# Optimization experiments

Measured on AMD Instinct MI355X. Metric: run time of the kernel, lower is better.

The kernel has to match this reference:

```python
import jax, jax.numpy as jnp
import numpy as np

N = 100000          # nodes
E = 1600000         # edges (before self-loops)
D_IN = 128          # graph.x feature dim
D_HID = 8           # hidden_dim = output_dim = 8 (hard-coded in __init__)
NUM_MASK = 10000    # int(0.1 * N), _mask_rate = 0.1
ATT_SLOPE = 0.2     # GATConv attention LeakyReLU slope
ACT_SLOPE = 0.01    # F.leaky_relu default slope


def setup_inputs() -> dict:
    key = jax.random.key(0)
    ks = jax.random.split(key, 16)
    x = jax.random.normal(ks[0], (N, D_IN), dtype=jnp.float32)
    edge_index = jax.random.randint(ks[1], (2, E), 0, N, dtype=jnp.int32)
    mask_nodes = jax.random.permutation(ks[2], N)[:NUM_MASK].astype(jnp.int32)
    s = lambda k, shape: jax.random.normal(k, shape, dtype=jnp.float32) * 0.1
    return {
        "x": x,
        "edge_index": edge_index,
        "mask_nodes": mask_nodes,
        "enc_mask_token": jnp.zeros((1, D_IN), dtype=jnp.float32),
        "enc_W": s(ks[3], (D_HID, D_IN)),
        "enc_a_src": s(ks[4], (D_HID,)),
        "enc_a_dst": s(ks[5], (D_HID,)),
        "enc_b": s(ks[6], (D_HID,)),
        "e2d_W": s(ks[7], (D_HID, D_HID)),
        "dec_W": s(ks[8], (D_IN, D_HID)),
        "dec_a_src": s(ks[9], (D_IN,)),
        "dec_a_dst": s(ks[10], (D_IN,)),
        "dec_b": s(ks[11], (D_IN,)),
    }


def gat_conv(x, W, a_src, a_dst, b, src, dst, n_nodes):
    """PyG GATConv, heads=1 (self-loops already appended to src/dst)."""
    h = x @ W.T                                  # [N, out]
    alpha_src = h @ a_src                        # [N]
    alpha_dst = h @ a_dst                        # [N]
    e = jax.nn.leaky_relu(alpha_src[src] + alpha_dst[dst], ATT_SLOPE)  # [E]
    # numerically-stable segment softmax over incoming edges per dst node
    m = jax.ops.segment_max(e, dst, num_segments=n_nodes)
    ex = jnp.exp(e - m[dst])
    denom = jax.ops.segment_sum(ex, dst, num_segments=n_nodes)
    alpha = ex / denom[dst]                      # [E]
    out = jax.ops.segment_sum(alpha[:, None] * h[src], dst, num_segments=n_nodes)
    return out + b


def reference(x, edge_index, mask_nodes, enc_mask_token,
              enc_W, enc_a_src, enc_a_dst, enc_b,
              e2d_W, dec_W, dec_a_src, dec_a_dst, dec_b):
    n = x.shape[0]
    # GATConv adds self-loops internally
    loops = jnp.arange(n, dtype=edge_index.dtype)
    src = jnp.concatenate([edge_index[0], loops])
    dst = jnp.concatenate([edge_index[1], loops])

    # encoding_mask_noise: out_x[mask]=0 then += enc_mask_token -> set to token
    use_x = x.at[mask_nodes].set(enc_mask_token[0])

    # encoder: GATConv(input_dim -> 8) + leaky_relu
    enc_rep = jax.nn.leaky_relu(
        gat_conv(use_x, enc_W, enc_a_src, enc_a_dst, enc_b, src, dst, n), ACT_SLOPE)

    rep = enc_rep @ e2d_W.T
    rep = rep.at[mask_nodes].set(0.0)            # re-mask before decoding

    # decoder: GATConv(8 -> input_dim) + leaky_relu
    recon = jax.nn.leaky_relu(
        gat_conv(rep, dec_W, dec_a_src, dec_a_dst, dec_b, src, dst, n), ACT_SLOPE)

    # cosine reconstruction loss on masked nodes (torch eps = 1e-8)
    x_init = x[mask_nodes]
    x_rec = recon[mask_nodes]
    eps = jnp.float32(1e-8)
    na = jnp.maximum(jnp.linalg.norm(x_rec, axis=-1), eps)
    nb = jnp.maximum(jnp.linalg.norm(x_init, axis=-1), eps)
    cos = jnp.sum(x_rec * x_init, axis=-1) / (na * nb)
    loss = 1.0 - jnp.mean(cos)
    return loss, enc_rep
```

## Files before the change

kernel.cpp:

```cpp
#include <hip/hip_runtime.h>

#define N_NODES 100000
#define N_EDGES 1600000
#define N_TOT   1700000
#define D_IN    128
#define D_H     8
#define N_MASK  10000

#define TS      256
#define NTE     391
#define CAPB    5760
#define TSD     64
#define NTD     157
#define CAPD    1536
#define NB_NODE 196
#define NB_BKT  831

__device__ __forceinline__ float lrelu(float v, float s){ return v > 0.f ? v : s*v; }

__device__ __forceinline__ float wave_sum(float v){
#pragma unroll
  for (int o = 32; o > 0; o >>= 1) v += __shfl_xor(v, o, 64);
  return v;
}

__global__ void k_ms(const int* __restrict__ mask_nodes, int* __restrict__ mask_slot,
                     const float* __restrict__ Wd, const float* __restrict__ a_src,
                     float* __restrict__ vvec){
  int i = blockIdx.x*blockDim.x + threadIdx.x;
  if (i < N_MASK) mask_slot[mask_nodes[i]] = i;
  if (blockIdx.x == 0 && threadIdx.x < D_H){
    float s = 0.f;
    for (int j = 0; j < D_IN; ++j) s += a_src[j] * Wd[j*D_H + threadIdx.x];
    vvec[threadIdx.x] = s;
  }
}

__global__ void __launch_bounds__(512) k_pre(
    const float* __restrict__ x, const float* __restrict__ token,
    const float* __restrict__ W, const float* __restrict__ a_src,
    const float* __restrict__ a_dst, const int* __restrict__ mask_slot,
    const int* __restrict__ ei,
    float* __restrict__ h1, float* __restrict__ as1, float* __restrict__ ad1,
    int* __restrict__ gcur_enc, int* __restrict__ gcur_dec,
    unsigned* __restrict__ be, unsigned* __restrict__ bd){
  __shared__ float smem[1104];
  if (blockIdx.x < NB_NODE){
    float* Ws = smem;
    float* sa = smem + D_H*D_IN;
    float* sd = sa + D_H;
    for (int t = threadIdx.x; t < D_H*D_IN; t += 512) Ws[t] = W[t];
    if (threadIdx.x < D_H)            sa[threadIdx.x] = a_src[threadIdx.x];
    else if (threadIdx.x < 2*D_H)     sd[threadIdx.x - D_H] = a_dst[threadIdx.x - D_H];
    __syncthreads();
    int wid = blockIdx.x*512 + threadIdx.x;
    if (wid >= N_NODES) return;
    const float* row = (mask_slot[wid] >= 0) ? token : (x + (size_t)wid*D_IN);
    float acc[D_H];
#pragma unroll
    for (int j = 0; j < D_H; ++j) acc[j] = 0.f;
#pragma unroll 8
    for (int i = 0; i < D_IN/4; ++i){
      float4 xc = *(const float4*)(row + 4*i);
#pragma unroll
      for (int j = 0; j < D_H; ++j){
        float4 wv = *(const float4*)(Ws + j*D_IN + 4*i);
        acc[j] += xc.x*wv.x + xc.y*wv.y + xc.z*wv.z + xc.w*wv.w;
      }
    }
    float as = 0.f, ad = 0.f;
#pragma unroll
    for (int j = 0; j < D_H; ++j){ as += acc[j]*sa[j]; ad += acc[j]*sd[j]; }
    float4* hp = (float4*)(h1 + (size_t)wid*D_H);
    hp[0] = make_float4(acc[0], acc[1], acc[2], acc[3]);
    hp[1] = make_float4(acc[4], acc[5], acc[6], acc[7]);
    as1[wid] = as; ad1[wid] = ad;
  } else {
    int* h_enc    = (int*)smem;
    int* base_enc = h_enc + NTE;
    int* h_dec    = base_enc + NTE;
    int* base_dec = h_dec + NTD;
    int tid = threadIdx.x;
    if (tid < NTE){ h_enc[tid] = 0; }
    if (tid < NTD){ h_dec[tid] = 0; }
    __syncthreads();
    int t0 = (blockIdx.x - NB_NODE)*2048;
    int s[4], d[4], sl[4];
#pragma unroll
    for (int k = 0; k < 4; ++k){
      int t = t0 + tid + k*512;
      s[k] = -1;
      if (t < N_TOT){
        if (t < N_EDGES){ s[k] = ei[t]; d[k] = ei[N_EDGES + t]; }
        else            { s[k] = t - N_EDGES; d[k] = s[k]; }
        sl[k] = mask_slot[d[k]];
        atomicAdd(&h_enc[d[k] >> 8], 1);
        if (sl[k] >= 0) atomicAdd(&h_dec[sl[k] >> 6], 1);
      }
    }
    __syncthreads();
    if (tid < NTE){ base_enc[tid] = atomicAdd(&gcur_enc[tid], h_enc[tid]); h_enc[tid] = 0; }
    if (tid < NTD){ base_dec[tid] = atomicAdd(&gcur_dec[tid], h_dec[tid]); h_dec[tid] = 0; }
    __syncthreads();
#pragma unroll
    for (int k = 0; k < 4; ++k){
      if (s[k] >= 0){
        int b = d[k] >> 8, loc = d[k] & 255;
        int idx = base_enc[b] + atomicAdd(&h_enc[b], 1);
        if (idx < CAPB) be[(size_t)b*CAPB + idx] = ((unsigned)s[k] << 8) | (unsigned)loc;
        if (sl[k] >= 0){
          int bs = sl[k] >> 6, locs = sl[k] & 63;
          int i2 = base_dec[bs] + atomicAdd(&h_dec[bs], 1);
          if (i2 < CAPD) bd[(size_t)bs*CAPD + i2] = ((unsigned)s[k] << 6) | (unsigned)locs;
        }
      }
    }
  }
}

__global__ void __launch_bounds__(512) k_agg_enc(const unsigned* __restrict__ be,
                          const int* __restrict__ gcur_enc,
                          const float* __restrict__ as1, const float* __restrict__ ad1,
                          const float* __restrict__ h1,
                          const float* __restrict__ enc_b, const float* __restrict__ e2dW,
                          const int* __restrict__ mask_slot, const float* __restrict__ v,
                          float* __restrict__ out_rep, float* __restrict__ rep,
                          float* __restrict__ ex2){
  __shared__ unsigned sorted[CAPB];
  __shared__ int hist[TS], off[TS], cur[TS];
  __shared__ float lad[TS];
  __shared__ float comb[TS*9];
  int tau = blockIdx.x, tid = threadIdx.x;
  int gb = tau*TS;
  if (tid < TS){
    hist[tid] = 0;
    int g = gb + tid; lad[tid] = (g < N_NODES) ? ad1[g] : 0.f;
  }
  __syncthreads();
  int n = min(gcur_enc[tau], CAPB);
  const unsigned* bb = be + (size_t)tau*CAPB;
  for (int i = tid; i < n; i += 512) atomicAdd(&hist[bb[i] & 255], 1);
  __syncthreads();
  if (tid < TS) off[tid] = hist[tid];
  __syncthreads();
#pragma unroll
  for (int s2 = 1; s2 < TS; s2 <<= 1){
    int vv = 0;
    if (tid < TS && tid >= s2) vv = off[tid - s2];
    __syncthreads();
    if (tid < TS) off[tid] += vv;
    __syncthreads();
  }
  if (tid < TS) cur[tid] = off[tid] - hist[tid];
  __syncthreads();
  for (int i = tid; i < n; i += 512){
    unsigned w = bb[i];
    int pos = atomicAdd(&cur[w & 255], 1);
    sorted[pos] = w;
  }
  __syncthreads();
  int c = tid & 255, half = tid >> 8;
  int start = off[c] - hist[c], deg = hist[c];
  int mid = start + ((deg + 1) >> 1), end = start + deg;
  int k0 = half ? mid : start, k1 = half ? end : mid;
  float adv = lad[c];
  float acc[9];
#pragma unroll
  for (int j = 0; j < 9; ++j) acc[j] = 0.f;
  int k = k0;
  for (; k + 2 <= k1; k += 2){
    unsigned w0 = sorted[k], w1 = sorted[k+1];
    int sA = w0 >> 8, sB = w1 >> 8;
    float asA = as1[sA], asB = as1[sB];
    float4 haA = *(const float4*)(h1 + (size_t)sA*D_H);
    float4 hbA = *(const float4*)(h1 + (size_t)sA*D_H + 4);
    float4 haB = *(const float4*)(h1 + (size_t)sB*D_H);
    float4 hbB = *(const float4*)(h1 + (size_t)sB*D_H + 4);
    float exA = __expf(lrelu(asA + adv, 0.2f));
    float exB = __expf(lrelu(asB + adv, 0.2f));
    acc[0] += exA*haA.x; acc[1] += exA*haA.y; acc[2] += exA*haA.z; acc[3] += exA*haA.w;
    acc[4] += exA*hbA.x; acc[5] += exA*hbA.y; acc[6] += exA*hbA.z; acc[7] += exA*hbA.w;
    acc[8] += exA;
    acc[0] += exB*haB.x; acc[1] += exB*haB.y; acc[2] += exB*haB.z; acc[3] += exB*haB.w;
    acc[4] += exB*hbB.x; acc[5] += exB*hbB.y; acc[6] += exB*hbB.z; acc[7] += exB*hbB.w;
    acc[8] += exB;
  }
  if (k < k1){
    unsigned w = sorted[k];
    int s = w >> 8;
    float as = as1[s];
    float4 ha = *(const float4*)(h1 + (size_t)s*D_H);
    float4 hb = *(const float4*)(h1 + (size_t)s*D_H + 4);
    float ex = __expf(lrelu(as + adv, 0.2f));
    acc[0] += ex*ha.x; acc[1] += ex*ha.y; acc[2] += ex*ha.z; acc[3] += ex*ha.w;
    acc[4] += ex*hb.x; acc[5] += ex*hb.y; acc[6] += ex*hb.z; acc[7] += ex*hb.w;
    acc[8] += ex;
  }
  if (half){
#pragma unroll
    for (int j = 0; j < 9; ++j) comb[c*9 + j] = acc[j];
  }
  __syncthreads();
  if (!half){
    int i = gb + c;
    if (i < N_NODES){
#pragma unroll
      for (int j = 0; j < 9; ++j) acc[j] += comb[c*9 + j];
      float inv = 1.0f / acc[8];
      float er[D_H];
#pragma unroll
      for (int j = 0; j < D_H; ++j){
        er[j] = lrelu(acc[j]*inv + enc_b[j], 0.01f);
        out_rep[(size_t)i*D_H + j] = er[j];
      }
      bool masked = mask_slot[i] >= 0;
      float as = 0.f;
      float rv[D_H];
#pragma unroll
      for (int kk = 0; kk < D_H; ++kk){
        float t = 0.f;
#pragma unroll
        for (int j = 0; j < D_H; ++j) t += er[j]*e2dW[kk*D_H + j];
        t = masked ? 0.f : t;
        rv[kk] = t;
        as += t * v[kk];
      }
      float4* rp = (float4*)(rep + (size_t)i*D_H);
      rp[0] = make_float4(rv[0], rv[1], rv[2], rv[3]);
      rp[1] = make_float4(rv[4], rv[5], rv[6], rv[7]);
      ex2[i] = __expf(lrelu(as, 0.2f));
    }
  }
}

__global__ void __launch_bounds__(512) k_agg_dec(const unsigned* __restrict__ bd,
                          const int* __restrict__ gcur_dec,
                          const float* __restrict__ ex2, const float* __restrict__ rep,
                          const float* __restrict__ Wd, const float* __restrict__ dec_b,
                          const int* __restrict__ mask_nodes, const float* __restrict__ x,
                          float* __restrict__ cos_sum, int* __restrict__ ticket,
                          float* __restrict__ out){
  __shared__ unsigned sorted[CAPD];
  __shared__ int hist[TSD], off[TSD], cur[TSD];
  __shared__ float comb[TSD*9];
  __shared__ float Wt[D_H*D_IN];
  __shared__ float wsum[8];
  int sg = blockIdx.x, tid = threadIdx.x;
  if (tid < TSD) hist[tid] = 0;
  for (int t = tid; t < D_H*D_IN; t += 512) Wt[(t & 7)*D_IN + (t >> 3)] = Wd[t];
  __syncthreads();
  int n = min(gcur_dec[sg], CAPD);
  const unsigned* bb = bd + (size_t)sg*CAPD;
  for (int i = tid; i < n; i += 512) atomicAdd(&hist[bb[i] & 63], 1);
  __syncthreads();
  if (tid < TSD) off[tid] = hist[tid];
  __syncthreads();
#pragma unroll
  for (int s2 = 1; s2 < TSD; s2 <<= 1){
    int vv = 0;
    if (tid < TSD && tid >= s2) vv = off[tid - s2];
    __syncthreads();
    if (tid < TSD) off[tid] += vv;
    __syncthreads();
  }
  if (tid < TSD) cur[tid] = off[tid] - hist[tid];
  __syncthreads();
  for (int i = tid; i < n; i += 512){
    unsigned w = bb[i];
    int pos = atomicAdd(&cur[w & 63], 1);
    sorted[pos] = w;
  }
  __syncthreads();
  int c = tid >> 3, part = tid & 7;
  int start = off[c] - hist[c], deg = hist[c], end = start + deg;
  float acc[9];
#pragma unroll
  for (int j = 0; j < 9; ++j) acc[j] = 0.f;
  int k = start + part;
  for (; k + 8 < end; k += 16){
    unsigned w0 = sorted[k], w1 = sorted[k+8];
    int sA = w0 >> 6, sB = w1 >> 6;
    float eA = ex2[sA], eB = ex2[sB];
    float4 raA = *(const float4*)(rep + (size_t)sA*D_H);
    float4 rbA = *(const float4*)(rep + (size_t)sA*D_H + 4);
    float4 raB = *(const float4*)(rep + (size_t)sB*D_H);
    float4 rbB = *(const float4*)(rep + (size_t)sB*D_H + 4);
    acc[0] += eA*raA.x; acc[1] += eA*raA.y; acc[2] += eA*raA.z; acc[3] += eA*raA.w;
    acc[4] += eA*rbA.x; acc[5] += eA*rbA.y; acc[6] += eA*rbA.z; acc[7] += eA*rbA.w;
    acc[8] += eA;
    acc[0] += eB*raB.x; acc[1] += eB*raB.y; acc[2] += eB*raB.z; acc[3] += eB*raB.w;
    acc[4] += eB*rbB.x; acc[5] += eB*rbB.y; acc[6] += eB*rbB.z; acc[7] += eB*rbB.w;
    acc[8] += eB;
  }
  if (k < end){
    unsigned w = sorted[k];
    int s = w >> 6;
    float E = ex2[s];
    float4 ra = *(const float4*)(rep + (size_t)s*D_H);
    float4 rb = *(const float4*)(rep + (size_t)s*D_H + 4);
    acc[0] += E*ra.x; acc[1] += E*ra.y; acc[2] += E*ra.z; acc[3] += E*ra.w;
    acc[4] += E*rb.x; acc[5] += E*rb.y; acc[6] += E*rb.z; acc[7] += E*rb.w;
    acc[8] += E;
  }
#pragma unroll
  for (int j = 0; j < 9; ++j){
    acc[j] += __shfl_xor(acc[j], 1, 64);
    acc[j] += __shfl_xor(acc[j], 2, 64);
    acc[j] += __shfl_xor(acc[j], 4, 64);
  }
  if (part == 0){
#pragma unroll
    for (int j = 0; j < 9; ++j) comb[c*9 + j] = acc[j];
  }
  __syncthreads();
  int wv = tid >> 6, lane = tid & 63;
  float accv = 0.f;
  for (int sl = wv; sl < TSD; sl += 8){
    int slot = sg*TSD + sl;
    if (slot >= N_MASK) break;
    const float* a = comb + sl*9;
    float inv = 1.0f / a[8];
    int node = mask_nodes[slot];
    float dot = 0.f, na = 0.f, nb = 0.f;
#pragma unroll
    for (int hh = 0; hh < 2; ++hh){
      int f = lane + 64*hh;
      float r = dec_b[f];
#pragma unroll
      for (int kk = 0; kk < D_H; ++kk) r += a[kk]*inv*Wt[kk*D_IN + f];
      r = lrelu(r, 0.01f);
      float xi = x[(size_t)node*D_IN + f];
      dot += r*xi; na += r*r; nb += xi*xi;
    }
    dot = wave_sum(dot); na = wave_sum(na); nb = wave_sum(nb);
    if (lane == 0) accv += dot / (fmaxf(sqrtf(na), 1e-8f)*fmaxf(sqrtf(nb), 1e-8f));
  }
  if (lane == 0) wsum[wv] = accv;
  __syncthreads();
  if (tid == 0){
    float b = 0.f;
#pragma unroll
    for (int q = 0; q < 8; ++q) b += wsum[q];
    atomicAdd(cos_sum, b);
    __threadfence();
    int t = atomicAdd(ticket, 1);
    if (t == gridDim.x - 1){
      float cc = atomicAdd(cos_sum, 0.0f);
      out[0] = 1.0f - cc / (float)N_MASK;
    }
  }
}

extern "C" void kernel_launch(void* const* d_in, const int* in_sizes, int n_in,
                              void* d_out, int out_size, void* d_ws, size_t ws_size,
                              hipStream_t stream){
  const float* x          = (const float*)d_in[0];
  const int*   ei         = (const int*)  d_in[1];
  const int*   mask_nodes = (const int*)  d_in[2];
  const float* token      = (const float*)d_in[3];
  const float* enc_W      = (const float*)d_in[4];
  const float* enc_as     = (const float*)d_in[5];
  const float* enc_ad     = (const float*)d_in[6];
  const float* enc_b      = (const float*)d_in[7];
  const float* e2d_W      = (const float*)d_in[8];
  const float* dec_W      = (const float*)d_in[9];
  const float* dec_as     = (const float*)d_in[10];
  const float* dec_b      = (const float*)d_in[12];
  float* out = (float*)d_out;

  char* w = (char*)d_ws;
  size_t off = 0;
  auto alloc = [&](size_t bytes)->char*{ char* p = w + off; off += (bytes + 255)/256*256; return p; };
  int*   gcur_enc = (int*)  alloc(NTE*4);
  int*   gcur_dec = (int*)  alloc(NTD*4);
  float* cos_sum  = (float*)alloc(4);
  int*   ticket   = (int*)  alloc(4);
  size_t zero_bytes = off;
  int*      mask_slot = (int*)     alloc((size_t)N_NODES*4);
  unsigned* be        = (unsigned*)alloc((size_t)NTE*CAPB*4);
  unsigned* bd        = (unsigned*)alloc((size_t)NTD*CAPD*4);
  float*    h1        = (float*)   alloc((size_t)N_NODES*D_H*4);
  float*    as1       = (float*)   alloc((size_t)N_NODES*4);
  float*    ad1       = (float*)   alloc((size_t)N_NODES*4);
  float*    rep       = (float*)   alloc((size_t)N_NODES*D_H*4);
  float*    ex2       = (float*)   alloc((size_t)N_NODES*4);
  float*    vvec      = (float*)   alloc(64);

  hipMemsetAsync(d_ws, 0, zero_bytes, stream);
  hipMemsetAsync(mask_slot, 0xFF, (size_t)N_NODES*4, stream);

  k_ms      <<<(N_MASK + 255)/256, 256, 0, stream>>>(mask_nodes, mask_slot, dec_W, dec_as, vvec);
  k_pre     <<<NB_NODE + NB_BKT, 512, 0, stream>>>(x, token, enc_W, enc_as, enc_ad, mask_slot,
                                                   ei, h1, as1, ad1, gcur_enc, gcur_dec, be, bd);
  k_agg_enc <<<NTE, 512, 0, stream>>>(be, gcur_enc, as1, ad1, h1, enc_b, e2d_W, mask_slot,
                                      vvec, out + 1, rep, ex2);
  k_agg_dec <<<NTD, 512, 0, stream>>>(bd, gcur_dec, ex2, rep, dec_W, dec_b, mask_nodes, x,
                                      cos_sum, ticket, out);
}
```

Measured before the change: 94.53 us.

## Split encoder projection across 8 lanes per node and replace memsets with init kernel

The encoder linear projection now assigns eight threads per node, each loading a 16-float slice of the row with coalesced float4 reads, then reduces the partial dot products with cross-lane shuffles. The block count for node work grows accordingly. Separately, the two hipMemsetAsync calls are replaced by a single small init kernel that sets mask_slot and the counters. This targets uncoalesced per-thread row reads and launch overhead, at the cost of more blocks and extra shuffles.

```diff
diff --git a/kernel.cpp b/kernel.cpp
--- a/kernel.cpp
+++ b/kernel.cpp
@@ -13,7 +13,7 @@
 #define TSD     64
 #define NTD     157
 #define CAPD    1536
-#define NB_NODE 196
+#define NB_NODE 1563
 #define NB_BKT  831
 
 __device__ __forceinline__ float lrelu(float v, float s){ return v > 0.f ? v : s*v; }
@@ -22,6 +22,18 @@
 #pragma unroll
   for (int o = 32; o > 0; o >>= 1) v += __shfl_xor(v, o, 64);
   return v;
+}
+
+__global__ void k_init(int* __restrict__ mask_slot, int* __restrict__ gcur_enc,
+                       int* __restrict__ gcur_dec, float* __restrict__ cos_sum,
+                       int* __restrict__ ticket){
+  int i = blockIdx.x*blockDim.x + threadIdx.x;
+  if (i < N_NODES) mask_slot[i] = -1;
+  if (blockIdx.x == 0){
+    if (threadIdx.x < NTE) gcur_enc[threadIdx.x] = 0;
+    if (threadIdx.x < NTD) gcur_dec[threadIdx.x] = 0;
+    if (threadIdx.x == 0){ cos_sum[0] = 0.f; ticket[0] = 0; }
+  }
 }
 
 __global__ void k_ms(const int* __restrict__ mask_nodes, int* __restrict__ mask_slot,
@@ -53,28 +65,46 @@
     if (threadIdx.x < D_H)            sa[threadIdx.x] = a_src[threadIdx.x];
     else if (threadIdx.x < 2*D_H)     sd[threadIdx.x - D_H] = a_dst[threadIdx.x - D_H];
     __syncthreads();
-    int wid = blockIdx.x*512 + threadIdx.x;
-    if (wid >= N_NODES) return;
-    const float* row = (mask_slot[wid] >= 0) ? token : (x + (size_t)wid*D_IN);
+    int p = threadIdx.x & 7;
+    int node = blockIdx.x*64 + (threadIdx.x >> 3);
+    if (node >= N_NODES) return;
+    const float* row = (mask_slot[node] >= 0) ? token : (x + (size_t)node*D_IN);
+    const float* rp = row + p*16;
+    float4 xa = *(const float4*)(rp);
+    float4 xb = *(const float4*)(rp + 4);
+    float4 xc = *(const float4*)(rp + 8);
+    float4 xd = *(const float4*)(rp + 12);
     float acc[D_H];
 #pragma unroll
-    for (int j = 0; j < D_H; ++j) acc[j] = 0.f;
-#pragma unroll 8
-    for (int i = 0; i < D_IN/4; ++i){
-      float4 xc = *(const float4*)(row + 4*i);
-#pragma unroll
-      for (int j = 0; j < D_H; ++j){
-        float4 wv = *(const float4*)(Ws + j*D_IN + 4*i);
-        acc[j] += xc.x*wv.x + xc.y*wv.y + xc.z*wv.z + xc.w*wv.w;
-      }
-    }
-    float as = 0.f, ad = 0.f;
-#pragma unroll
-    for (int j = 0; j < D_H; ++j){ as += acc[j]*sa[j]; ad += acc[j]*sd[j]; }
-    float4* hp = (float4*)(h1 + (size_t)wid*D_H);
-    hp[0] = make_float4(acc[0], acc[1], acc[2], acc[3]);
-    hp[1] = make_float4(acc[4], acc[5], acc[6], acc[7]);
-    as1[wid] = as; ad1[wid] = ad;
+    for (int j = 0; j < D_H; ++j){
+      const float* wj = Ws + j*D_IN + p*16;
+      float4 wa = *(const float4*)(wj);
+      float4 wb = *(const float4*)(wj + 4);
+      float4 wc = *(const float4*)(wj + 8);
+      float4 wd = *(const float4*)(wj + 12);
+      acc[j] = xa.x*wa.x + xa.y*wa.y + xa.z*wa.z + xa.w*wa.w
+             + xb.x*wb.x + xb.y*wb.y + xb.z*wb.z + xb.w*wb.w
+             + xc.x*wc.x + xc.y*wc.y + xc.z*wc.z + xc.w*wc.w
+             + xd.x*wd.x + xd.y*wd.y + xd.z*wd.z + xd.w*wd.w;
+    }
+#pragma unroll
+    for (int j = 0; j < D_H; ++j){
+      acc[j] += __shfl_xor(acc[j], 1, 64);
+      acc[j] += __shfl_xor(acc[j], 2, 64);
+      acc[j] += __shfl_xor(acc[j], 4, 64);
+    }
+    h1[(size_t)node*D_H + p] = acc[p];
+    if (p == 0){
+      float as = 0.f;
+#pragma unroll
+      for (int j = 0; j < D_H; ++j) as += acc[j]*sa[j];
+      as1[node] = as;
+    } else if (p == 1){
+      float ad = 0.f;
+#pragma unroll
+      for (int j = 0; j < D_H; ++j) ad += acc[j]*sd[j];
+      ad1[node] = ad;
+    }
   } else {
     int* h_enc    = (int*)smem;
     int* base_enc = h_enc + NTE;
@@ -375,7 +405,6 @@
   int*   gcur_dec = (int*)  alloc(NTD*4);
   float* cos_sum  = (float*)alloc(4);
   int*   ticket   = (int*)  alloc(4);
-  size_t zero_bytes = off;
   int*      mask_slot = (int*)     alloc((size_t)N_NODES*4);
   unsigned* be        = (unsigned*)alloc((size_t)NTE*CAPB*4);
   unsigned* bd        = (unsigned*)alloc((size_t)NTD*CAPD*4);
@@ -386,9 +415,7 @@
   float*    ex2       = (float*)   alloc((size_t)N_NODES*4);
   float*    vvec      = (float*)   alloc(64);
 
-  hipMemsetAsync(d_ws, 0, zero_bytes, stream);
-  hipMemsetAsync(mask_slot, 0xFF, (size_t)N_NODES*4, stream);
-
+  k_init    <<<(N_NODES + 511)/512, 512, 0, stream>>>(mask_slot, gcur_enc, gcur_dec, cos_sum, ticket);
   k_ms      <<<(N_MASK + 255)/256, 256, 0, stream>>>(mask_nodes, mask_slot, dec_W, dec_as, vvec);
   k_pre     <<<NB_NODE + NB_BKT, 512, 0, stream>>>(x, token, enc_W, enc_as, enc_ad, mask_slot,
                                                    ei, h1, as1, ad1, gcur_enc, gcur_dec, be, bd);
```

Result: slower. 98.29 us (+4.0%).

## Replace block-local histogram bucketing with direct padded global atomics

Applied to the files above, without the earlier changes.

The edge-bucketing blocks no longer build a per-block shared-memory histogram and reserve ranges with one global atomic per bucket. Instead each edge does its own global atomicAdd on a bucket counter, and the counters are padded to 16 ints apart to avoid false sharing. The two memsets are replaced by a single init kernel. This removes two block barriers and the two-pass structure, but raises global atomic traffic to about 1.7M contended atomics on 391 counters.

```diff
diff --git a/kernel.cpp b/kernel.cpp
--- a/kernel.cpp
+++ b/kernel.cpp
@@ -15,6 +15,7 @@
 #define CAPD    1536
 #define NB_NODE 196
 #define NB_BKT  831
+#define CPAD    16
 
 __device__ __forceinline__ float lrelu(float v, float s){ return v > 0.f ? v : s*v; }
 
@@ -22,6 +23,16 @@
 #pragma unroll
   for (int o = 32; o > 0; o >>= 1) v += __shfl_xor(v, o, 64);
   return v;
+}
+
+__global__ void k_init(int* __restrict__ mask_slot, int* __restrict__ gcur_enc,
+                       int* __restrict__ gcur_dec, float* __restrict__ cos_sum,
+                       int* __restrict__ ticket){
+  int i = blockIdx.x*blockDim.x + threadIdx.x;
+  if (i < N_NODES) mask_slot[i] = -1;
+  if (i < NTE*CPAD) gcur_enc[i] = 0;
+  if (i < NTD*CPAD) gcur_dec[i] = 0;
+  if (i == 0){ cos_sum[0] = 0.f; ticket[0] = 0; }
 }
 
 __global__ void k_ms(const int* __restrict__ mask_nodes, int* __restrict__ mask_slot,
@@ -44,7 +55,7 @@
     float* __restrict__ h1, float* __restrict__ as1, float* __restrict__ ad1,
     int* __restrict__ gcur_enc, int* __restrict__ gcur_dec,
     unsigned* __restrict__ be, unsigned* __restrict__ bd){
-  __shared__ float smem[1104];
+  __shared__ float smem[D_H*D_IN + 2*D_H];
   if (blockIdx.x < NB_NODE){
     float* Ws = smem;
     float* sa = smem + D_H*D_IN;
@@ -76,42 +87,22 @@
     hp[1] = make_float4(acc[4], acc[5], acc[6], acc[7]);
     as1[wid] = as; ad1[wid] = ad;
   } else {
-    int* h_enc    = (int*)smem;
-    int* base_enc = h_enc + NTE;
-    int* h_dec    = base_enc + NTE;
-    int* base_dec = h_dec + NTD;
-    int tid = threadIdx.x;
-    if (tid < NTE){ h_enc[tid] = 0; }
-    if (tid < NTD){ h_dec[tid] = 0; }
-    __syncthreads();
     int t0 = (blockIdx.x - NB_NODE)*2048;
-    int s[4], d[4], sl[4];
 #pragma unroll
     for (int k = 0; k < 4; ++k){
-      int t = t0 + tid + k*512;
-      s[k] = -1;
+      int t = t0 + threadIdx.x + k*512;
       if (t < N_TOT){
-        if (t < N_EDGES){ s[k] = ei[t]; d[k] = ei[N_EDGES + t]; }
-        else            { s[k] = t - N_EDGES; d[k] = s[k]; }
-        sl[k] = mask_slot[d[k]];
-        atomicAdd(&h_enc[d[k] >> 8], 1);
-        if (sl[k] >= 0) atomicAdd(&h_dec[sl[k] >> 6], 1);
-      }
-    }
-    __syncthreads();
-    if (tid < NTE){ base_enc[tid] = atomicAdd(&gcur_enc[tid], h_enc[tid]); h_enc[tid] = 0; }
-    if (tid < NTD){ base_dec[tid] = atomicAdd(&gcur_dec[tid], h_dec[tid]); h_dec[tid] = 0; }
-    __syncthreads();
-#pragma unroll
-    for (int k = 0; k < 4; ++k){
-      if (s[k] >= 0){
-        int b = d[k] >> 8, loc = d[k] & 255;
-        int idx = base_enc[b] + atomicAdd(&h_enc[b], 1);
-        if (idx < CAPB) be[(size_t)b*CAPB + idx] = ((unsigned)s[k] << 8) | (unsigned)loc;
-        if (sl[k] >= 0){
-          int bs = sl[k] >> 6, locs = sl[k] & 63;
-          int i2 = base_dec[bs] + atomicAdd(&h_dec[bs], 1);
-          if (i2 < CAPD) bd[(size_t)bs*CAPD + i2] = ((unsigned)s[k] << 6) | (unsigned)locs;
+        int s, d;
+        if (t < N_EDGES){ s = ei[t]; d = ei[N_EDGES + t]; }
+        else            { s = t - N_EDGES; d = s; }
+        int sl = mask_slot[d];
+        int b = d >> 8, loc = d & 255;
+        int idx = atomicAdd(&gcur_enc[b*CPAD], 1);
+        if (idx < CAPB) be[(size_t)b*CAPB + idx] = ((unsigned)s << 8) | (unsigned)loc;
+        if (sl >= 0){
+          int bs = sl >> 6, locs = sl & 63;
+          int i2 = atomicAdd(&gcur_dec[bs*CPAD], 1);
+          if (i2 < CAPD) bd[(size_t)bs*CAPD + i2] = ((unsigned)s << 6) | (unsigned)locs;
         }
       }
     }
@@ -137,7 +128,7 @@
     int g = gb + tid; lad[tid] = (g < N_NODES) ? ad1[g] : 0.f;
   }
   __syncthreads();
-  int n = min(gcur_enc[tau], CAPB);
+  int n = min(gcur_enc[tau*CPAD], CAPB);
   const unsigned* bb = be + (size_t)tau*CAPB;
   for (int i = tid; i < n; i += 512) atomicAdd(&hist[bb[i] & 255], 1);
   __syncthreads();
@@ -249,7 +240,7 @@
   if (tid < TSD) hist[tid] = 0;
   for (int t = tid; t < D_H*D_IN; t += 512) Wt[(t & 7)*D_IN + (t >> 3)] = Wd[t];
   __syncthreads();
-  int n = min(gcur_dec[sg], CAPD);
+  int n = min(gcur_dec[sg*CPAD], CAPD);
   const unsigned* bb = bd + (size_t)sg*CAPD;
   for (int i = tid; i < n; i += 512) atomicAdd(&hist[bb[i] & 63], 1);
   __syncthreads();
@@ -371,11 +362,10 @@
   char* w = (char*)d_ws;
   size_t off = 0;
   auto alloc = [&](size_t bytes)->char*{ char* p = w + off; off += (bytes + 255)/256*256; return p; };
-  int*   gcur_enc = (int*)  alloc(NTE*4);
-  int*   gcur_dec = (int*)  alloc(NTD*4);
+  int*   gcur_enc = (int*)  alloc((size_t)NTE*CPAD*4);
+  int*   gcur_dec = (int*)  alloc((size_t)NTD*CPAD*4);
   float* cos_sum  = (float*)alloc(4);
   int*   ticket   = (int*)  alloc(4);
-  size_t zero_bytes = off;
   int*      mask_slot = (int*)     alloc((size_t)N_NODES*4);
   unsigned* be        = (unsigned*)alloc((size_t)NTE*CAPB*4);
   unsigned* bd        = (unsigned*)alloc((size_t)NTD*CAPD*4);
@@ -386,9 +376,7 @@
   float*    ex2       = (float*)   alloc((size_t)N_NODES*4);
   float*    vvec      = (float*)   alloc(64);
 
-  hipMemsetAsync(d_ws, 0, zero_bytes, stream);
-  hipMemsetAsync(mask_slot, 0xFF, (size_t)N_NODES*4, stream);
-
+  k_init    <<<(N_NODES + 511)/512, 512, 0, stream>>>(mask_slot, gcur_enc, gcur_dec, cos_sum, ticket);
   k_ms      <<<(N_MASK + 255)/256, 256, 0, stream>>>(mask_nodes, mask_slot, dec_W, dec_as, vvec);
   k_pre     <<<NB_NODE + NB_BKT, 512, 0, stream>>>(x, token, enc_W, enc_as, enc_ad, mask_slot,
                                                    ei, h1, as1, ad1, gcur_enc, gcur_dec, be, bd);
```

Result: slower. 205.2 us (+117.1%).

## Handle self-loops analytically, replace memsets with init kernel, unroll gather by four

Applied to the files above, without the earlier changes.

Self-loop edges are no longer written into the bucket arrays. The encoder adds each node's self-loop term directly after its edge reduction, and the decoder adds 1 to the softmax denominator, since the masked rep is zero. Two hipMemsetAsync calls become one small init kernel, and the encoder gather loop is unrolled from two edges per step to four to expose more memory-level parallelism. This cuts the bucketing and sorting work and one launch of overhead. The decoder shortcut depends on the self-loop contribution for a masked node being exactly an exp of 1 with a zero rep value.

```diff
diff --git a/kernel.cpp b/kernel.cpp
--- a/kernel.cpp
+++ b/kernel.cpp
@@ -2,7 +2,6 @@
 
 #define N_NODES 100000
 #define N_EDGES 1600000
-#define N_TOT   1700000
 #define D_IN    128
 #define D_H     8
 #define N_MASK  10000
@@ -14,7 +13,8 @@
 #define NTD     157
 #define CAPD    1536
 #define NB_NODE 196
-#define NB_BKT  831
+#define EPB     2048
+#define NB_BKT  782
 
 __device__ __forceinline__ float lrelu(float v, float s){ return v > 0.f ? v : s*v; }
 
@@ -22,6 +22,16 @@
 #pragma unroll
   for (int o = 32; o > 0; o >>= 1) v += __shfl_xor(v, o, 64);
   return v;
+}
+
+__global__ void k_init(int* __restrict__ mask_slot, int* __restrict__ gcur_enc,
+                       int* __restrict__ gcur_dec, float* __restrict__ cos_sum,
+                       int* __restrict__ ticket){
+  int i = blockIdx.x*blockDim.x + threadIdx.x;
+  if (i < N_NODES) mask_slot[i] = -1;
+  if (i < NTE) gcur_enc[i] = 0;
+  if (i < NTD) gcur_dec[i] = 0;
+  if (i == 0){ cos_sum[0] = 0.f; ticket[0] = 0; }
 }
 
 __global__ void k_ms(const int* __restrict__ mask_nodes, int* __restrict__ mask_slot,
@@ -44,10 +54,10 @@
     float* __restrict__ h1, float* __restrict__ as1, float* __restrict__ ad1,
     int* __restrict__ gcur_enc, int* __restrict__ gcur_dec,
     unsigned* __restrict__ be, unsigned* __restrict__ bd){
-  __shared__ float smem[1104];
+  __shared__ int smem[1104];
   if (blockIdx.x < NB_NODE){
-    float* Ws = smem;
-    float* sa = smem + D_H*D_IN;
+    float* Ws = (float*)smem;
+    float* sa = Ws + D_H*D_IN;
     float* sd = sa + D_H;
     for (int t = threadIdx.x; t < D_H*D_IN; t += 512) Ws[t] = W[t];
     if (threadIdx.x < D_H)            sa[threadIdx.x] = a_src[threadIdx.x];
@@ -76,23 +86,22 @@
     hp[1] = make_float4(acc[4], acc[5], acc[6], acc[7]);
     as1[wid] = as; ad1[wid] = ad;
   } else {
-    int* h_enc    = (int*)smem;
+    int* h_enc    = smem;
     int* base_enc = h_enc + NTE;
     int* h_dec    = base_enc + NTE;
     int* base_dec = h_dec + NTD;
     int tid = threadIdx.x;
-    if (tid < NTE){ h_enc[tid] = 0; }
-    if (tid < NTD){ h_dec[tid] = 0; }
-    __syncthreads();
-    int t0 = (blockIdx.x - NB_NODE)*2048;
+    if (tid < NTE) h_enc[tid] = 0;
+    if (tid < NTD) h_dec[tid] = 0;
+    __syncthreads();
+    int t0 = (blockIdx.x - NB_NODE)*EPB;
     int s[4], d[4], sl[4];
 #pragma unroll
     for (int k = 0; k < 4; ++k){
       int t = t0 + tid + k*512;
       s[k] = -1;
-      if (t < N_TOT){
-        if (t < N_EDGES){ s[k] = ei[t]; d[k] = ei[N_EDGES + t]; }
-        else            { s[k] = t - N_EDGES; d[k] = s[k]; }
+      if (t < N_EDGES){
+        s[k] = ei[t]; d[k] = ei[N_EDGES + t];
         sl[k] = mask_slot[d[k]];
         atomicAdd(&h_enc[d[k] >> 8], 1);
         if (sl[k] >= 0) atomicAdd(&h_dec[sl[k] >> 6], 1);
@@ -167,26 +176,7 @@
   float acc[9];
 #pragma unroll
   for (int j = 0; j < 9; ++j) acc[j] = 0.f;
-  int k = k0;
-  for (; k + 2 <= k1; k += 2){
-    unsigned w0 = sorted[k], w1 = sorted[k+1];
-    int sA = w0 >> 8, sB = w1 >> 8;
-    float asA = as1[sA], asB = as1[sB];
-    float4 haA = *(const float4*)(h1 + (size_t)sA*D_H);
-    float4 hbA = *(const float4*)(h1 + (size_t)sA*D_H + 4);
-    float4 haB = *(const float4*)(h1 + (size_t)sB*D_H);
-    float4 hbB = *(const float4*)(h1 + (size_t)sB*D_H + 4);
-    float exA = __expf(lrelu(asA + adv, 0.2f));
-    float exB = __expf(lrelu(asB + adv, 0.2f));
-    acc[0] += exA*haA.x; acc[1] += exA*haA.y; acc[2] += exA*haA.z; acc[3] += exA*haA.w;
-    acc[4] += exA*hbA.x; acc[5] += exA*hbA.y; acc[6] += exA*hbA.z; acc[7] += exA*hbA.w;
-    acc[8] += exA;
-    acc[0] += exB*haB.x; acc[1] += exB*haB.y; acc[2] += exB*haB.z; acc[3] += exB*haB.w;
-    acc[4] += exB*hbB.x; acc[5] += exB*hbB.y; acc[6] += exB*hbB.z; acc[7] += exB*hbB.w;
-    acc[8] += exB;
-  }
-  if (k < k1){
-    unsigned w = sorted[k];
+  auto edge1 = [&](unsigned w){
     int s = w >> 8;
     float as = as1[s];
     float4 ha = *(const float4*)(h1 + (size_t)s*D_H);
@@ -195,7 +185,31 @@
     acc[0] += ex*ha.x; acc[1] += ex*ha.y; acc[2] += ex*ha.z; acc[3] += ex*ha.w;
     acc[4] += ex*hb.x; acc[5] += ex*hb.y; acc[6] += ex*hb.z; acc[7] += ex*hb.w;
     acc[8] += ex;
-  }
+  };
+  int k = k0;
+  for (; k + 4 <= k1; k += 4){
+    unsigned w0 = sorted[k], w1 = sorted[k+1], w2 = sorted[k+2], w3 = sorted[k+3];
+    int s0 = w0 >> 8, s1 = w1 >> 8, s2 = w2 >> 8, s3 = w3 >> 8;
+    float a0 = as1[s0], a1 = as1[s1], a2 = as1[s2], a3 = as1[s3];
+    float4 h0a = *(const float4*)(h1 + (size_t)s0*D_H), h0b = *(const float4*)(h1 + (size_t)s0*D_H + 4);
+    float4 h1a = *(const float4*)(h1 + (size_t)s1*D_H), h1b = *(const float4*)(h1 + (size_t)s1*D_H + 4);
+    float4 h2a = *(const float4*)(h1 + (size_t)s2*D_H), h2b = *(const float4*)(h1 + (size_t)s2*D_H + 4);
+    float4 h3a = *(const float4*)(h1 + (size_t)s3*D_H), h3b = *(const float4*)(h1 + (size_t)s3*D_H + 4);
+    float e0 = __expf(lrelu(a0 + adv, 0.2f));
+    float e1 = __expf(lrelu(a1 + adv, 0.2f));
+    float e2 = __expf(lrelu(a2 + adv, 0.2f));
+    float e3 = __expf(lrelu(a3 + adv, 0.2f));
+    acc[0] += e0*h0a.x + e1*h1a.x + e2*h2a.x + e3*h3a.x;
+    acc[1] += e0*h0a.y + e1*h1a.y + e2*h2a.y + e3*h3a.y;
+    acc[2] += e0*h0a.z + e1*h1a.z + e2*h2a.z + e3*h3a.z;
+    acc[3] += e0*h0a.w + e1*h1a.w + e2*h2a.w + e3*h3a.w;
+    acc[4] += e0*h0b.x + e1*h1b.x + e2*h2b.x + e3*h3b.x;
+    acc[5] += e0*h0b.y + e1*h1b.y + e2*h2b.y + e3*h3b.y;
+    acc[6] += e0*h0b.z + e1*h1b.z + e2*h2b.z + e3*h3b.z;
+    acc[7] += e0*h0b.w + e1*h1b.w + e2*h2b.w + e3*h3b.w;
+    acc[8] += e0 + e1 + e2 + e3;
+  }
+  for (; k < k1; ++k) edge1(sorted[k]);
   if (half){
 #pragma unroll
     for (int j = 0; j < 9; ++j) comb[c*9 + j] = acc[j];
@@ -206,6 +220,14 @@
     if (i < N_NODES){
 #pragma unroll
       for (int j = 0; j < 9; ++j) acc[j] += comb[c*9 + j];
+      {
+        float exs = __expf(lrelu(as1[i] + adv, 0.2f));
+        float4 ha = *(const float4*)(h1 + (size_t)i*D_H);
+        float4 hb = *(const float4*)(h1 + (size_t)i*D_H + 4);
+        acc[0] += exs*ha.x; acc[1] += exs*ha.y; acc[2] += exs*ha.z; acc[3] += exs*ha.w;
+        acc[4] += exs*hb.x; acc[5] += exs*hb.y; acc[6] += exs*hb.z; acc[7] += exs*hb.w;
+        acc[8] += exs;
+      }
       float inv = 1.0f / acc[8];
       float er[D_H];
 #pragma unroll
@@ -309,6 +331,7 @@
     acc[j] += __shfl_xor(acc[j], 4, 64);
   }
   if (part == 0){
+    acc[8] += 1.0f;
 #pragma unroll
     for (int j = 0; j < 9; ++j) comb[c*9 + j] = acc[j];
   }
@@ -375,7 +398,6 @@
   int*   gcur_dec = (int*)  alloc(NTD*4);
   float* cos_sum  = (float*)alloc(4);
   int*   ticket   = (int*)  alloc(4);
-  size_t zero_bytes = off;
   int*      mask_slot = (int*)     alloc((size_t)N_NODES*4);
   unsigned* be        = (unsigned*)alloc((size_t)NTE*CAPB*4);
   unsigned* bd        = (unsigned*)alloc((size_t)NTD*CAPD*4);
@@ -386,9 +408,7 @@
   float*    ex2       = (float*)   alloc((size_t)N_NODES*4);
   float*    vvec      = (float*)   alloc(64);
 
-  hipMemsetAsync(d_ws, 0, zero_bytes, stream);
-  hipMemsetAsync(mask_slot, 0xFF, (size_t)N_NODES*4, stream);
-
+  k_init    <<<(N_NODES + 511)/512, 512, 0, stream>>>(mask_slot, gcur_enc, gcur_dec, cos_sum, ticket);
   k_ms      <<<(N_MASK + 255)/256, 256, 0, stream>>>(mask_nodes, mask_slot, dec_W, dec_as, vvec);
   k_pre     <<<NB_NODE + NB_BKT, 512, 0, stream>>>(x, token, enc_W, enc_as, enc_ad, mask_slot,
                                                    ei, h1, as1, ad1, gcur_enc, gcur_dec, be, bd);
```

New measurement: 90.97 us. 1.04x faster.
